# Kernel tuning notes

Hardware: AMD Instinct MI355X
Metric: run time of the kernel (lower is better)

The kernel has to match this reference:

```python
import jax, jax.numpy as jnp
import numpy as np
import math

S = 5   # num_states
D = 16  # observation_dim
F = 4   # transition_feature_dim
H = 2 * S  # transition net hidden


def setup_inputs() -> dict:
    key = jax.random.key(0)
    ks = jax.random.split(key, 10)
    B, T = 256, 4096
    observations = jax.random.normal(ks[0], (B, T, D), dtype=jnp.float32)
    transition_features = jax.random.normal(ks[1], (B, T, F), dtype=jnp.float32)
    # GaussianEmission params
    means = jax.random.normal(ks[2], (S, D), dtype=jnp.float32) * 0.1
    log_vars = jnp.zeros((S, D), dtype=jnp.float32)
    # HMM params
    log_initial = jnp.zeros((S,), dtype=jnp.float32)
    transition_bias = (jnp.eye(S) * 2.0 + jnp.ones((S, S)) * 0.1).astype(jnp.float32)
    # per-source-state transition nets: Linear(F,H)-Tanh-Linear(H,S)
    W1 = jax.random.normal(ks[3], (S, H, F), dtype=jnp.float32) * (1.0 / math.sqrt(F))
    b1 = jnp.zeros((S, H), dtype=jnp.float32)
    W2 = jax.random.normal(ks[4], (S, S, H), dtype=jnp.float32) * (1.0 / math.sqrt(H))
    b2 = jnp.zeros((S, S), dtype=jnp.float32)
    return {
        "observations": observations,
        "transition_features": transition_features,
        "means": means,
        "log_vars": log_vars,
        "log_initial": log_initial,
        "transition_bias": transition_bias,
        "W1": W1, "b1": b1, "W2": W2, "b2": b2,
    }


def _emission_log_prob(obs, means, log_vars):
    # diagonal Gaussian, expanded quadratic form to avoid [B,T,S,D] intermediate
    inv_v = jnp.exp(-log_vars)                              # [S,D]
    quad = (
        jnp.einsum('btd,sd->bts', obs * obs, inv_v)
        - 2.0 * jnp.einsum('btd,sd->bts', obs, means * inv_v)
        + jnp.sum(means * means * inv_v, axis=-1)           # [S]
    )
    const = D * math.log(2 * math.pi) + jnp.sum(log_vars, axis=-1)  # [S]
    return -0.5 * (const + quad)                            # [B,T,S]


def _io_log_transitions(feat, W1, b1, W2, b2, transition_bias):
    # feat: [B,T,F] -> log transition matrices [B,T,S,S] (row i = source state)
    h = jnp.tanh(jnp.einsum('btf,ihf->btih', feat, W1) + b1)        # [B,T,S,H]
    logits = jnp.einsum('btih,ioh->btio', h, W2) + b2 + transition_bias  # [B,T,S,S]
    probs = jax.nn.softmax(logits, axis=-1)
    return jnp.log(probs + 1e-10)


def reference(observations, transition_features, means, log_vars,
              log_initial, transition_bias, W1, b1, W2, b2):
    log_emis = _emission_log_prob(observations, means, log_vars)    # [B,T,S]
    log_init = jax.nn.log_softmax(log_initial)                      # [S]
    alpha0 = log_init + log_emis[:, 0, :]                           # [B,S]

    # transitions used at steps t=1..T-1
    log_trans = _io_log_transitions(transition_features[:, 1:], W1, b1, W2, b2,
                                    transition_bias)                # [B,T-1,S,S]

    lt_tm = jnp.swapaxes(log_trans, 0, 1)                           # [T-1,B,S,S]
    le_tm = jnp.swapaxes(log_emis[:, 1:, :], 0, 1)                  # [T-1,B,S]

    def step(alpha, xs):
        lt, le = xs
        alpha_new = jax.nn.logsumexp(alpha[:, :, None] + lt, axis=1) + le
        return alpha_new, alpha_new

    alpha_T, alphas = jax.lax.scan(step, alpha0, (lt_tm, le_tm))
    all_alpha = jnp.concatenate([alpha0[None], alphas], axis=0)     # [T,B,S]
    all_alpha = jnp.swapaxes(all_alpha, 0, 1)                       # [B,T,S]
    log_likelihood = jax.nn.logsumexp(alpha_T, axis=-1)             # [B]
    return log_likelihood, all_alpha
```

## Files before the change

### kernel.cpp

```cpp
#include <hip/hip_runtime.h>
#include <math.h>


namespace {

constexpr int kS = 5, kD = 16, kB = 256, kT = 4096;
constexpr int kC = 8, kNC = 512;
constexpr int kTile = 256, kCPT = 32;
constexpr int kG = 16, kNG = 32;

constexpr float kL2E = 1.4426950408889634f;
constexpr float kLn2 = 0.6931471805599453f;

constexpr int L_QA  = 0;
constexpr int L_QB  = 80;
constexpr int L_QC  = 160;
constexpr int L_LN  = 168;
constexpr int L_W1H = 176;
constexpr int L_B1  = 276;
constexpr int L_W2H = 336;
constexpr int P_TOT = 544;
constexpr int P_RSV = 1024;

typedef __fp16 half2_t __attribute__((ext_vector_type(2)));

#if __has_builtin(__builtin_amdgcn_exp2f)
__device__ __forceinline__ float ex2(float x) { return __builtin_amdgcn_exp2f(x); }
#else
__device__ __forceinline__ float ex2(float x) { return exp2f(x); }
#endif
#if __has_builtin(__builtin_amdgcn_logf)
__device__ __forceinline__ float lg2(float x) { return __builtin_amdgcn_logf(x); }
#else
__device__ __forceinline__ float lg2(float x) { return __log2f(x); }
#endif

__device__ __forceinline__ unsigned pkh(float a, float b) {
  return __builtin_bit_cast(unsigned, __builtin_amdgcn_cvt_pkrtz(a, b));
}

#if __has_builtin(__builtin_amdgcn_fdot2)
__device__ __forceinline__ float fdot2u(unsigned w, unsigned x, float acc) {
  return __builtin_amdgcn_fdot2(__builtin_bit_cast(half2_t, w),
                                __builtin_bit_cast(half2_t, x), acc, false);
}
#else
__device__ __forceinline__ float fdot2u(unsigned w, unsigned x, float acc) {
  const half2_t hw = __builtin_bit_cast(half2_t, w);
  const half2_t hx = __builtin_bit_cast(half2_t, x);
  return acc + (float)hw.x * (float)hx.x + (float)hw.y * (float)hx.y;
}
#endif

__device__ __forceinline__ float max5(float a0, float a1, float a2, float a3, float a4) {
  return fmaxf(fmaxf(fmaxf(a0, a1), fmaxf(a2, a3)), a4);
}

__device__ __forceinline__ unsigned bf16bits(float x) {
  unsigned u = __float_as_uint(x);
  return (u + 0x7fffu + ((u >> 16) & 1u)) >> 16;
}

__device__ __forceinline__ unsigned cvtpk(float a, float b) {
  unsigned r;
  asm("v_cvt_pk_bf16_f32 %0, %1, %2" : "=v"(r) : "v"(a), "v"(b));
  return r;
}

__device__ __forceinline__ int swcol(int row, int e) {
  return (e + 11 * (row >> 3) + (row & 7)) & 15;
}

__global__ void k_prep(const float* __restrict__ means, const float* __restrict__ lv,
                       const float* __restrict__ linit, const float* __restrict__ tbias,
                       const float* __restrict__ W1g, const float* __restrict__ b1g,
                       const float* __restrict__ W2g, const float* __restrict__ b2g,
                       float* __restrict__ P) {
  const int tid = threadIdx.x;
  if (tid < 80) {
    const float iv = __expf(-lv[tid]);
    P[L_QA + tid] = -0.5f * kL2E * iv;
    P[L_QB + tid] = kL2E * means[tid] * iv;
  }
  if (tid >= 80 && tid < 85) {
    const int s = tid - 80;
    float acc = 0.f;
#pragma unroll
    for (int d = 0; d < 16; ++d) {
      const float lvv = lv[s * 16 + d], mm = means[s * 16 + d];
      acc += lvv + mm * mm * __expf(-lvv);
    }
    P[L_QC + s] = -0.5f * kL2E * (29.406033062549525f + acc);
    const float l0 = linit[0], l1 = linit[1], l2 = linit[2], l3 = linit[3],
                l4 = linit[4];
    const float m = max5(l0, l1, l2, l3, l4);
    const float se = __expf(l0 - m) + __expf(l1 - m) + __expf(l2 - m) +
                     __expf(l3 - m) + __expf(l4 - m);
    P[L_LN + s] = kL2E * (linit[s] - (m + __logf(se)));
  }
  if (tid < 100) {
    const int i = tid / 20, rem = tid - i * 20, h = rem >> 1, part = rem & 1;
    const int base = (i * 10 + h) * 4 + part * 2;
    P[L_W1H + tid] = __uint_as_float(pkh((2.0f * kL2E) * W1g[base],
                                         (2.0f * kL2E) * W1g[base + 1]));
  }
  if (tid < 60) {
    const int r = tid / 12, h = tid - r * 12;
    P[L_B1 + tid] = (h < 10) ? (2.0f * kL2E) * b1g[r * 10 + h] : 0.f;
  }
  if (tid < 200) {
    const int r = tid >> 3, s = tid & 7;
    float v = 0.f;
    if (s < 5) {
      v = __uint_as_float(pkh(-2.0f * kL2E * W2g[r * 10 + 2 * s],
                              -2.0f * kL2E * W2g[r * 10 + 2 * s + 1]));
    } else if (s == 5) {
      float sw = 0.f;
#pragma unroll
      for (int hh = 0; hh < 10; ++hh) sw += W2g[r * 10 + hh];
      v = kL2E * (b2g[r] + tbias[r] + sw);
    }
    P[L_W2H + tid] = v;
  }
  if (tid < 3) { P[165 + tid] = 0.f; P[173 + tid] = 0.f; }
  if (tid < 8) P[536 + tid] = 0.f;
}

__device__ __forceinline__ void buildE(const float* __restrict__ obs,
                                       const float* __restrict__ feat,
                                       const float* __restrict__ p,
                                       size_t t, float E[25], float& c) {
  float o[16], o2[16];
  {
    const float4* o4 = reinterpret_cast<const float4*>(obs + t * kD);
    const float4 v0 = o4[0], v1 = o4[1], v2 = o4[2], v3 = o4[3];
    o[0] = v0.x; o[1] = v0.y; o[2] = v0.z; o[3] = v0.w;
    o[4] = v1.x; o[5] = v1.y; o[6] = v1.z; o[7] = v1.w;
    o[8] = v2.x; o[9] = v2.y; o[10] = v2.z; o[11] = v2.w;
    o[12] = v3.x; o[13] = v3.y; o[14] = v3.z; o[15] = v3.w;
  }
#pragma unroll
  for (int d = 0; d < 16; ++d) o2[d] = o[d] * o[d];
  float le[5];
#pragma unroll
  for (int s = 0; s < 5; ++s) {
    float acc = p[L_QC + s];
#pragma unroll
    for (int dq = 0; dq < 4; ++dq) {
      const float4 qa = *reinterpret_cast<const float4*>(p + L_QA + s * 16 + dq * 4);
      const float4 qb = *reinterpret_cast<const float4*>(p + L_QB + s * 16 + dq * 4);
      acc = fmaf(o2[dq * 4 + 0], qa.x, acc); acc = fmaf(o[dq * 4 + 0], qb.x, acc);
      acc = fmaf(o2[dq * 4 + 1], qa.y, acc); acc = fmaf(o[dq * 4 + 1], qb.y, acc);
      acc = fmaf(o2[dq * 4 + 2], qa.z, acc); acc = fmaf(o[dq * 4 + 2], qb.z, acc);
      acc = fmaf(o2[dq * 4 + 3], qa.w, acc); acc = fmaf(o[dq * 4 + 3], qb.w, acc);
    }
    le[s] = acc;
  }
  c = max5(le[0], le[1], le[2], le[3], le[4]);
  float eml[5];
#pragma unroll
  for (int j = 0; j < 5; ++j) eml[j] = ex2(le[j] - c);
  const float4 f = *reinterpret_cast<const float4*>(feat + t * 4);
  const unsigned f01 = pkh(f.x, f.y), f23 = pkh(f.z, f.w);
#pragma unroll
  for (int i = 0; i < 5; ++i) {
    const float4 bA = *reinterpret_cast<const float4*>(p + L_B1 + i * 12);
    const float4 bB = *reinterpret_cast<const float4*>(p + L_B1 + i * 12 + 4);
    const float2 bC = *reinterpret_cast<const float2*>(p + L_B1 + i * 12 + 8);
    const uint4 wa = *reinterpret_cast<const uint4*>(p + L_W1H + i * 20);
    const uint4 wb = *reinterpret_cast<const uint4*>(p + L_W1H + i * 20 + 4);
    const uint4 wc = *reinterpret_cast<const uint4*>(p + L_W1H + i * 20 + 8);
    const uint4 wd = *reinterpret_cast<const uint4*>(p + L_W1H + i * 20 + 12);
    const uint4 we = *reinterpret_cast<const uint4*>(p + L_W1H + i * 20 + 16);
    const float r0 = __builtin_amdgcn_rcpf(ex2(fdot2u(wa.y, f23, fdot2u(wa.x, f01, bA.x))) + 1.f);
    const float r1 = __builtin_amdgcn_rcpf(ex2(fdot2u(wa.w, f23, fdot2u(wa.z, f01, bA.y))) + 1.f);
    const float r2 = __builtin_amdgcn_rcpf(ex2(fdot2u(wb.y, f23, fdot2u(wb.x, f01, bA.z))) + 1.f);
    const float r3 = __builtin_amdgcn_rcpf(ex2(fdot2u(wb.w, f23, fdot2u(wb.z, f01, bA.w))) + 1.f);
    const float r4 = __builtin_amdgcn_rcpf(ex2(fdot2u(wc.y, f23, fdot2u(wc.x, f01, bB.x))) + 1.f);
    const float r5 = __builtin_amdgcn_rcpf(ex2(fdot2u(wc.w, f23, fdot2u(wc.z, f01, bB.y))) + 1.f);
    const float r6 = __builtin_amdgcn_rcpf(ex2(fdot2u(wd.y, f23, fdot2u(wd.x, f01, bB.z))) + 1.f);
    const float r7 = __builtin_amdgcn_rcpf(ex2(fdot2u(wd.w, f23, fdot2u(wd.z, f01, bB.w))) + 1.f);
    const float r8 = __builtin_amdgcn_rcpf(ex2(fdot2u(we.y, f23, fdot2u(we.x, f01, bC.x))) + 1.f);
    const float r9 = __builtin_amdgcn_rcpf(ex2(fdot2u(we.w, f23, fdot2u(we.z, f01, bC.y))) + 1.f);
    const unsigned h01 = pkh(r0, r1), h23 = pkh(r2, r3), h45 = pkh(r4, r5),
                   h67 = pkh(r6, r7), h89 = pkh(r8, r9);
    float eg[5], se = 0.f;
#pragma unroll
    for (int j = 0; j < 5; ++j) {
      const uint4 v = *reinterpret_cast<const uint4*>(p + L_W2H + (i * 5 + j) * 8);
      const uint2 v2 = *reinterpret_cast<const uint2*>(p + L_W2H + (i * 5 + j) * 8 + 4);
      float acc = __uint_as_float(v2.y);
      acc = fdot2u(v.x, h01, acc);
      acc = fdot2u(v.y, h23, acc);
      acc = fdot2u(v.z, h45, acc);
      acc = fdot2u(v.w, h67, acc);
      acc = fdot2u(v2.x, h89, acc);
      eg[j] = ex2(acc);
      se += eg[j];
    }
    const float rs = __builtin_amdgcn_rcpf(se);
#pragma unroll
    for (int j = 0; j < 5; ++j) E[i * 5 + j] = eg[j] * rs * eml[j];
  }
}

__device__ __forceinline__ void buildE0(const float* __restrict__ obs,
                                        const float* __restrict__ p, int b,
                                        float E[25], float& c) {
  float o[16], o2[16];
  {
    const float4* o4 = reinterpret_cast<const float4*>(obs + (size_t)b * kT * kD);
    const float4 v0 = o4[0], v1 = o4[1], v2 = o4[2], v3 = o4[3];
    o[0] = v0.x; o[1] = v0.y; o[2] = v0.z; o[3] = v0.w;
    o[4] = v1.x; o[5] = v1.y; o[6] = v1.z; o[7] = v1.w;
    o[8] = v2.x; o[9] = v2.y; o[10] = v2.z; o[11] = v2.w;
    o[12] = v3.x; o[13] = v3.y; o[14] = v3.z; o[15] = v3.w;
  }
#pragma unroll
  for (int d = 0; d < 16; ++d) o2[d] = o[d] * o[d];
  float v[5];
#pragma unroll
  for (int s = 0; s < 5; ++s) {
    float acc = p[L_QC + s];
#pragma unroll
    for (int dq = 0; dq < 4; ++dq) {
      const float4 qa = *reinterpret_cast<const float4*>(p + L_QA + s * 16 + dq * 4);
      const float4 qb = *reinterpret_cast<const float4*>(p + L_QB + s * 16 + dq * 4);
      acc = fmaf(o2[dq * 4 + 0], qa.x, acc); acc = fmaf(o[dq * 4 + 0], qb.x, acc);
      acc = fmaf(o2[dq * 4 + 1], qa.y, acc); acc = fmaf(o[dq * 4 + 1], qb.y, acc);
      acc = fmaf(o2[dq * 4 + 2], qa.z, acc); acc = fmaf(o[dq * 4 + 2], qb.z, acc);
      acc = fmaf(o2[dq * 4 + 3], qa.w, acc); acc = fmaf(o[dq * 4 + 3], qb.w, acc);
    }
    v[s] = acc + p[L_LN + s];
  }
  c = max5(v[0], v[1], v[2], v[3], v[4]);
  float e5[5];
#pragma unroll
  for (int j = 0; j < 5; ++j) e5[j] = 0.2f * ex2(v[j] - c);
#pragma unroll
  for (int i = 0; i < 5; ++i)
#pragma unroll
    for (int j = 0; j < 5; ++j) E[i * 5 + j] = e5[j];
}

template <bool STORE_E>
__global__ __launch_bounds__(kTile, 4) void k_build(
    const float* __restrict__ obs, const float* __restrict__ feat,
    const float* __restrict__ P, float* __restrict__ Rg,
    uint4* __restrict__ wsE) {
  __shared__ __align__(16) float p[P_TOT];
  __shared__ unsigned sw[kTile * 16];
  if (threadIdx.x < P_TOT / 4)
    reinterpret_cast<float4*>(p)[threadIdx.x] =
        reinterpret_cast<const float4*>(P)[threadIdx.x];
  __syncthreads();
  const int b = blockIdx.y, tile = blockIdx.x, tid = threadIdx.x;
  const int t = tile * kTile + tid;
  const size_t gt = (size_t)b * kT + t;
  float E[25], c;
  if (t == 0) buildE0(obs, p, b, E, c);
  else buildE(obs, feat, p, gt, E, c);
  unsigned w[14];
  w[0] = cvtpk(E[0], E[1]);   w[1] = cvtpk(E[2], E[3]);
  w[2] = cvtpk(E[4], E[5]);   w[3] = cvtpk(E[6], E[7]);
  w[4] = cvtpk(E[8], E[9]);   w[5] = cvtpk(E[10], E[11]);
  w[6] = cvtpk(E[12], E[13]); w[7] = cvtpk(E[14], E[15]);
  w[8] = cvtpk(E[16], E[17]); w[9] = cvtpk(E[18], E[19]);
  w[10] = cvtpk(E[20], E[21]); w[11] = cvtpk(E[22], E[23]);
  {
    const unsigned cb = __float_as_uint(c);
    w[12] = bf16bits(E[24]) | (cb << 16);
    w[13] = cb >> 16;
  }
  if (STORE_E) {
    uint4* wp = wsE + gt * 4;
    wp[0] = make_uint4(w[0], w[1], w[2], w[3]);
    wp[1] = make_uint4(w[4], w[5], w[6], w[7]);
    wp[2] = make_uint4(w[8], w[9], w[10], w[11]);
    wp[3] = make_uint4(w[12], w[13], 0u, 0u);
  }
  {
    const int base = tid * 16;
#pragma unroll
    for (int e = 0; e < 14; ++e) sw[base + swcol(tid, e)] = w[e];
  }
  __syncthreads();
  const int chunk = tid >> 3, ri = tid & 7;
  float R[5], sc;
  {
    const int row = chunk * 8, base = row * 16, cb = 11 * chunk;
#pragma unroll
    for (int m = 0; m < 5; ++m) {
      const int sl = ri * 5 + m, widx = sl >> 1;
      const unsigned d = sw[base + ((widx + cb) & 15)];
      R[m] = __uint_as_float((sl & 1) ? (d & 0xffff0000u) : (d << 16));
    }
    const unsigned d12 = sw[base + ((12 + cb) & 15)];
    const unsigned d13 = sw[base + ((13 + cb) & 15)];
    sc = __uint_as_float((d12 >> 16) | (d13 << 16));
  }
#pragma unroll 1
  for (int k = 1; k < 8; ++k) {
    const int row = chunk * 8 + k, base = row * 16, cb = 11 * chunk + k;
    unsigned d[14];
#pragma unroll
    for (int e = 0; e < 14; ++e) d[e] = sw[base + ((e + cb) & 15)];
    float Ek[25];
#pragma unroll
    for (int q = 0; q < 12; ++q) {
      Ek[2 * q]     = __uint_as_float(d[q] << 16);
      Ek[2 * q + 1] = __uint_as_float(d[q] & 0xffff0000u);
    }
    Ek[24] = __uint_as_float(d[12] << 16);
    sc += __uint_as_float((d[12] >> 16) | (d[13] << 16));
    float nR[5];
#pragma unroll
    for (int j = 0; j < 5; ++j) {
      float acc = R[0] * Ek[j];
      acc = fmaf(R[1], Ek[5 + j], acc);
      acc = fmaf(R[2], Ek[10 + j], acc);
      acc = fmaf(R[3], Ek[15 + j], acc);
      acc = fmaf(R[4], Ek[20 + j], acc);
      nR[j] = acc;
    }
#pragma unroll
    for (int j = 0; j < 5; ++j) R[j] = nR[j];
    if ((k & 1) == 0 || k == 7) {
      float rm = (ri < 5) ? max5(R[0], R[1], R[2], R[3], R[4]) : 0.f;
      rm = fmaxf(rm, __shfl_xor(rm, 1, 8));
      rm = fmaxf(rm, __shfl_xor(rm, 2, 8));
      rm = fmaxf(rm, __shfl_xor(rm, 4, 8));
      rm = fmaxf(rm, 1e-30f);
      const float r = __builtin_amdgcn_rcpf(rm);
#pragma unroll
      for (int j = 0; j < 5; ++j) R[j] *= r;
      sc += lg2(rm);
    }
  }
  if (ri < 5) {
    float* outr = Rg + ((size_t)b * kNC + tile * kCPT + chunk) * 28 + ri * 5;
#pragma unroll
    for (int m = 0; m < 5; ++m) outr[m] = R[m];
    if (ri == 0) outr[25] = sc;
  }
}


__device__ __forceinline__ void matmat5(float R[25], const float E[25]) {
#pragma unroll
  for (int i = 0; i < 5; ++i) {
    const float r0 = R[i * 5 + 0], r1 = R[i * 5 + 1], r2 = R[i * 5 + 2];
    const float r3 = R[i * 5 + 3], r4 = R[i * 5 + 4];
#pragma unroll
    for (int j = 0; j < 5; ++j) {
      float acc = r0 * E[j];
      acc = fmaf(r1, E[5 + j], acc);
      acc = fmaf(r2, E[10 + j], acc);
      acc = fmaf(r3, E[15 + j], acc);
      acc = fmaf(r4, E[20 + j], acc);
      R[i * 5 + j] = acc;
    }
  }
}

__device__ __forceinline__ void rescale25a(float R[25], float& sc) {
  float m = R[0];
#pragma unroll
  for (int e = 1; e < 25; ++e) m = fmaxf(m, R[e]);
  m = fmaxf(m, 1e-30f);
  const float r = __builtin_amdgcn_rcpf(m);
#pragma unroll
  for (int e = 0; e < 25; ++e) R[e] *= r;
  sc += lg2(m);
}

__device__ __forceinline__ void vecmat5(float a[5], const float M[25]) {
  float o[5];
#pragma unroll
  for (int j = 0; j < 5; ++j) {
    float acc = a[0] * M[j];
    acc = fmaf(a[1], M[5 + j], acc);
    acc = fmaf(a[2], M[10 + j], acc);
    acc = fmaf(a[3], M[15 + j], acc);
    acc = fmaf(a[4], M[20 + j], acc);
    o[j] = acc;
  }
#pragma unroll
  for (int j = 0; j < 5; ++j) a[j] = o[j];
}

__device__ __forceinline__ void rescale5(float a[5], float& ls) {
  const float m = fmaxf(max5(a[0], a[1], a[2], a[3], a[4]), 1e-30f);
  const float r = __builtin_amdgcn_rcpf(m);
#pragma unroll
  for (int j = 0; j < 5; ++j) a[j] *= r;
  ls += lg2(m);
}

__global__ __launch_bounds__(256) void k_scan(const float* __restrict__ Rg,
                                              float* __restrict__ start,
                                              float* __restrict__ out) {
  __shared__ float sR[kNC * 32];
  __shared__ float sP[kNG * 28];
  __shared__ float sA[kNG * 8];
  const int b = blockIdx.x, tid = threadIdx.x;
#pragma unroll
  for (int r = 0; r < 2; ++r) {
    const int rec = r * 256 + tid;
    const float4* src = reinterpret_cast<const float4*>(Rg + ((size_t)b * kNC + rec) * 28);
    float4 q[7];
#pragma unroll
    for (int i = 0; i < 7; ++i) q[i] = src[i];
    const float* v = reinterpret_cast<const float*>(q);
    const int base = rec * 32, off = rec + (rec >> 4);
#pragma unroll
    for (int e = 0; e < 26; ++e) sR[base + ((off + e) & 31)] = v[e];
  }
  __syncthreads();
  if (tid < kNG) {
    const int g = tid;
    float P[25], psc;
    {
      const int rec = g * kG, base = rec * 32, off = rec + (rec >> 4);
#pragma unroll
      for (int e = 0; e < 25; ++e) P[e] = sR[base + ((off + e) & 31)];
      psc = sR[base + ((off + 25) & 31)];
    }
#pragma unroll 1
    for (int k = 1; k < kG; ++k) {
      const int rec = g * kG + k, base = rec * 32, off = rec + (rec >> 4);
      float M[25];
#pragma unroll
      for (int e = 0; e < 25; ++e) M[e] = sR[base + ((off + e) & 31)];
      psc += sR[base + ((off + 25) & 31)];
      matmat5(P, M);
      if (k & 1) rescale25a(P, psc);
    }
#pragma unroll
    for (int e = 0; e < 25; ++e) sP[g * 28 + e] = P[e];
    sP[g * 28 + 25] = psc;
  }
  __syncthreads();
  if (tid == 0) {
    float a[5] = {1.f, 1.f, 1.f, 1.f, 1.f};
    float ls = 0.f;
#pragma unroll 1
    for (int g = 0; g < kNG; ++g) {
#pragma unroll
      for (int s = 0; s < 5; ++s) sA[g * 8 + s] = a[s];
      sA[g * 8 + 5] = ls;
      float M[25];
#pragma unroll
      for (int e = 0; e < 25; ++e) M[e] = sP[g * 28 + e];
      vecmat5(a, M);
      ls += sP[g * 28 + 25];
      rescale5(a, ls);
    }
    out[b] = (lg2(a[0] + a[1] + a[2] + a[3] + a[4]) + ls) * kLn2;
  }
  __syncthreads();
  if (tid < kNG) {
    const int g = tid;
    float a[5], ls;
#pragma unroll
    for (int s = 0; s < 5; ++s) a[s] = sA[g * 8 + s];
    ls = sA[g * 8 + 5];
#pragma unroll 1
    for (int k = 0; k < kG; ++k) {
      const int cc = g * kG + k;
      float* st = start + ((size_t)b * kNC + cc) * 8;
      reinterpret_cast<float4*>(st)[0] = make_float4(a[0], a[1], a[2], a[3]);
      reinterpret_cast<float4*>(st)[1] = make_float4(a[4], ls, 0.f, 0.f);
      const int base = cc * 32, off = cc + (cc >> 4);
      float M[25];
#pragma unroll
      for (int e = 0; e < 25; ++e) M[e] = sR[base + ((off + e) & 31)];
      ls += sR[base + ((off + 25) & 31)];
      vecmat5(a, M);
      rescale5(a, ls);
    }
  }
}

__global__ __launch_bounds__(256) void k_alpha_a(const uint4* __restrict__ wsE,
                                                 const float* __restrict__ start,
                                                 float* __restrict__ outp) {
  const int gc = blockIdx.x * 256 + threadIdx.x;
  const int b = gc >> 9, cc = gc & (kNC - 1);
  const float* st = start + (size_t)gc * 8;
  const float4 s0 = reinterpret_cast<const float4*>(st)[0];
  const float4 s1 = reinterpret_cast<const float4*>(st)[1];
  float a[5] = {s0.x, s0.y, s0.z, s0.w, s1.x};
  float ls = s1.y;
  float ov[40];
  const uint4* ep = wsE + ((size_t)b * kT + (size_t)cc * kC) * 4;
#pragma unroll
  for (int k = 0; k < 8; ++k) {
    uint4 q0 = ep[k * 4], q1 = ep[k * 4 + 1], q2 = ep[k * 4 + 2], q3 = ep[k * 4 + 3];
    unsigned d[14] = {q0.x, q0.y, q0.z, q0.w, q1.x, q1.y, q1.z, q1.w,
                      q2.x, q2.y, q2.z, q2.w, q3.x, q3.y};
    float E[25];
#pragma unroll
    for (int q = 0; q < 12; ++q) {
      E[2 * q]     = __uint_as_float(d[q] << 16);
      E[2 * q + 1] = __uint_as_float(d[q] & 0xffff0000u);
    }
    E[24] = __uint_as_float(d[12] << 16);
    const float cst = __uint_as_float((d[12] >> 16) | (d[13] << 16));
    float o[5];
#pragma unroll
    for (int j = 0; j < 5; ++j) {
      float acc = a[0] * E[j];
      acc = fmaf(a[1], E[5 + j], acc);
      acc = fmaf(a[2], E[10 + j], acc);
      acc = fmaf(a[3], E[15 + j], acc);
      acc = fmaf(a[4], E[20 + j], acc);
      o[j] = acc;
    }
    ls += cst;
    float L[5];
#pragma unroll
    for (int j = 0; j < 5; ++j) L[j] = lg2(o[j]);
#pragma unroll
    for (int j = 0; j < 5; ++j) ov[k * 5 + j] = (L[j] + ls) * kLn2;
    const float lm = max5(L[0], L[1], L[2], L[3], L[4]);
    const float m = fmaxf(max5(o[0], o[1], o[2], o[3], o[4]), 1e-30f);
    const float r = __builtin_amdgcn_rcpf(m);
#pragma unroll
    for (int j = 0; j < 5; ++j) a[j] = o[j] * r;
    ls += lm;
  }
  float4* w = reinterpret_cast<float4*>(outp + kB + ((size_t)b * kT + (size_t)cc * kC) * kS);
#pragma unroll
  for (int q = 0; q < 10; ++q)
    w[q] = make_float4(ov[q * 4], ov[q * 4 + 1], ov[q * 4 + 2], ov[q * 4 + 3]);
}

}

extern "C" void kernel_launch(void* const* d_in, const int* in_sizes, int n_in,
                              void* d_out, int out_size, void* d_ws, size_t ws_size,
                              hipStream_t stream) {
  (void)in_sizes; (void)n_in; (void)out_size; (void)ws_size;
  const float* obs   = (const float*)d_in[0];
  const float* feat  = (const float*)d_in[1];
  const float* means = (const float*)d_in[2];
  const float* lv    = (const float*)d_in[3];
  const float* linit = (const float*)d_in[4];
  const float* tbias = (const float*)d_in[5];
  const float* W1g   = (const float*)d_in[6];
  const float* b1g   = (const float*)d_in[7];
  const float* W2g   = (const float*)d_in[8];
  const float* b2g   = (const float*)d_in[9];
  float* out = (float*)d_out;

  float* P     = (float*)d_ws;
  float* Rg    = P + P_RSV;
  float* start = Rg + (size_t)kB * kNC * 28;
  uint4* wsE   = reinterpret_cast<uint4*>(start + (size_t)kB * kNC * 8);

  k_prep<<<1, 256, 0, stream>>>(means, lv, linit, tbias, W1g, b1g, W2g, b2g, P);
  dim3 gridB(kT / kTile, kB);
  k_build<true><<<gridB, kTile, 0, stream>>>(obs, feat, P, Rg, wsE);
  k_scan<<<kB, 256, 0, stream>>>(Rg, start, out);
  k_alpha_a<<<(kB * kNC) / 256, 256, 0, stream>>>(wsE, start, out);
}
```

Measured before the change: 108.3 us.

## Split alpha output chunks in half using stored mid-chunk transfer products

k_build now also writes the partial 4-step transfer product of each 8-step chunk to a new workspace buffer. k_alpha_a launches twice as many threads, each emitting 4 timesteps. Second-half threads jump to their start state with that stored half-chunk matrix, or by replaying 4 steps if workspace is too small. This shortens each thread's serial dependency chain and raises parallelism, at the cost of extra global writes in k_build and extra workspace.

```diff
diff --git a/kernel.cpp b/kernel.cpp
--- a/kernel.cpp
+++ b/kernel.cpp
@@ -247,7 +247,7 @@
 __global__ __launch_bounds__(kTile, 4) void k_build(
     const float* __restrict__ obs, const float* __restrict__ feat,
     const float* __restrict__ P, float* __restrict__ Rg,
-    uint4* __restrict__ wsE) {
+    uint4* __restrict__ wsE, float* __restrict__ Rhg) {
   __shared__ __align__(16) float p[P_TOT];
   __shared__ unsigned sw[kTile * 16];
   if (threadIdx.x < P_TOT / 4)
@@ -336,6 +336,12 @@
       for (int j = 0; j < 5; ++j) R[j] *= r;
       sc += lg2(rm);
     }
+    if (k == 3 && Rhg != nullptr && ri < 5) {
+      float* hr = Rhg + ((size_t)b * kNC + tile * kCPT + chunk) * 28 + ri * 5;
+#pragma unroll
+      for (int m = 0; m < 5; ++m) hr[m] = R[m];
+      if (ri == 0) hr[25] = sc;
+    }
   }
   if (ri < 5) {
     float* outr = Rg + ((size_t)b * kNC + tile * kCPT + chunk) * 28 + ri * 5;
@@ -395,6 +401,18 @@
 #pragma unroll
   for (int j = 0; j < 5; ++j) a[j] *= r;
   ls += lg2(m);
+}
+
+__device__ __forceinline__ void loadRec(const float* __restrict__ base, size_t rec,
+                                        float M[25], float& msc) {
+  const float4* src = reinterpret_cast<const float4*>(base + rec * 28);
+  float4 q[7];
+#pragma unroll
+  for (int i = 0; i < 7; ++i) q[i] = src[i];
+  const float* v = reinterpret_cast<const float*>(q);
+#pragma unroll
+  for (int e = 0; e < 25; ++e) M[e] = v[e];
+  msc = v[25];
 }
 
 __global__ __launch_bounds__(256) void k_scan(const float* __restrict__ Rg,
@@ -484,18 +502,50 @@
 
 __global__ __launch_bounds__(256) void k_alpha_a(const uint4* __restrict__ wsE,
                                                  const float* __restrict__ start,
+                                                 const float* __restrict__ Rhg,
                                                  float* __restrict__ outp) {
-  const int gc = blockIdx.x * 256 + threadIdx.x;
-  const int b = gc >> 9, cc = gc & (kNC - 1);
-  const float* st = start + (size_t)gc * 8;
+  const int gcc = blockIdx.x * 256 + threadIdx.x;
+  const int b = gcc >> 10;
+  const int rem = gcc & 1023;
+  const int h = rem >> 9;
+  const int cc = rem & 511;
+  const float* st = start + ((size_t)b * kNC + cc) * 8;
   const float4 s0 = reinterpret_cast<const float4*>(st)[0];
   const float4 s1 = reinterpret_cast<const float4*>(st)[1];
   float a[5] = {s0.x, s0.y, s0.z, s0.w, s1.x};
   float ls = s1.y;
-  float ov[40];
-  const uint4* ep = wsE + ((size_t)b * kT + (size_t)cc * kC) * 4;
-#pragma unroll
-  for (int k = 0; k < 8; ++k) {
+  if (h) {
+    if (Rhg != nullptr) {
+      float M[25], msc;
+      loadRec(Rhg, (size_t)b * kNC + cc, M, msc);
+      vecmat5(a, M);
+      ls += msc;
+      rescale5(a, ls);
+    } else {
+      const uint4* pp = wsE + ((size_t)b * kT + (size_t)cc * kC) * 4;
+#pragma unroll
+      for (int k = 0; k < 4; ++k) {
+        uint4 q0 = pp[k * 4], q1 = pp[k * 4 + 1], q2 = pp[k * 4 + 2], q3 = pp[k * 4 + 3];
+        unsigned d[14] = {q0.x, q0.y, q0.z, q0.w, q1.x, q1.y, q1.z, q1.w,
+                          q2.x, q2.y, q2.z, q2.w, q3.x, q3.y};
+        float E[25];
+#pragma unroll
+        for (int q = 0; q < 12; ++q) {
+          E[2 * q]     = __uint_as_float(d[q] << 16);
+          E[2 * q + 1] = __uint_as_float(d[q] & 0xffff0000u);
+        }
+        E[24] = __uint_as_float(d[12] << 16);
+        vecmat5(a, E);
+        ls += __uint_as_float((d[12] >> 16) | (d[13] << 16));
+        rescale5(a, ls);
+      }
+    }
+  }
+  const size_t t0 = (size_t)cc * kC + (size_t)h * 4;
+  float ov[20];
+  const uint4* ep = wsE + ((size_t)b * kT + t0) * 4;
+#pragma unroll
+  for (int k = 0; k < 4; ++k) {
     uint4 q0 = ep[k * 4], q1 = ep[k * 4 + 1], q2 = ep[k * 4 + 2], q3 = ep[k * 4 + 3];
     unsigned d[14] = {q0.x, q0.y, q0.z, q0.w, q1.x, q1.y, q1.z, q1.w,
                       q2.x, q2.y, q2.z, q2.w, q3.x, q3.y};
@@ -530,9 +580,9 @@
     for (int j = 0; j < 5; ++j) a[j] = o[j] * r;
     ls += lm;
   }
-  float4* w = reinterpret_cast<float4*>(outp + kB + ((size_t)b * kT + (size_t)cc * kC) * kS);
-#pragma unroll
-  for (int q = 0; q < 10; ++q)
+  float4* w = reinterpret_cast<float4*>(outp + kB + ((size_t)b * kT + t0) * kS);
+#pragma unroll
+  for (int q = 0; q < 5; ++q)
     w[q] = make_float4(ov[q * 4], ov[q * 4 + 1], ov[q * 4 + 2], ov[q * 4 + 3]);
 }
 
@@ -541,7 +591,7 @@
 extern "C" void kernel_launch(void* const* d_in, const int* in_sizes, int n_in,
                               void* d_out, int out_size, void* d_ws, size_t ws_size,
                               hipStream_t stream) {
-  (void)in_sizes; (void)n_in; (void)out_size; (void)ws_size;
+  (void)in_sizes; (void)n_in; (void)out_size;
   const float* obs   = (const float*)d_in[0];
   const float* feat  = (const float*)d_in[1];
   const float* means = (const float*)d_in[2];
@@ -558,10 +608,15 @@
   float* Rg    = P + P_RSV;
   float* start = Rg + (size_t)kB * kNC * 28;
   uint4* wsE   = reinterpret_cast<uint4*>(start + (size_t)kB * kNC * 8);
+  float* Rhf   = reinterpret_cast<float*>(wsE) + (size_t)kB * kT * 16;
+  const size_t needB = ((size_t)P_RSV + (size_t)kB * kNC * 28 +
+                        (size_t)kB * kNC * 8 + (size_t)kB * kNC * 28) * 4 +
+                       (size_t)kB * kT * 64;
+  float* Rhg = (ws_size >= needB) ? Rhf : nullptr;
 
   k_prep<<<1, 256, 0, stream>>>(means, lv, linit, tbias, W1g, b1g, W2g, b2g, P);
   dim3 gridB(kT / kTile, kB);
-  k_build<true><<<gridB, kTile, 0, stream>>>(obs, feat, P, Rg, wsE);
+  k_build<true><<<gridB, kTile, 0, stream>>>(obs, feat, P, Rg, wsE, Rhg);
   k_scan<<<kB, 256, 0, stream>>>(Rg, start, out);
-  k_alpha_a<<<(kB * kNC) / 256, 256, 0, stream>>>(wsE, start, out);
-}
+  k_alpha_a<<<(kB * kNC * 2) / 256, 256, 0, stream>>>(wsE, start, Rhg, out);
+}
```

Result: slower. 117.0 us (+8.1%).

## Reduce each chunk's 5x5 transition products in one thread with doubled tiles

Applied to the files above, without the earlier changes.

The tile size goes from 256 to 512 timesteps, and chunks per tile go from 32 to 64. The per-chunk product of 8 emission-transition matrices changes mapping: before, 8 lanes each carried one row and shared a max via shuffles; now a single thread holds the full 5x5 matrix and rescales it with a local max. Results go out as contiguous float4 stores. This removes the cross-lane shuffles and the idle lanes (3 of every 8), but only 64 of 512 threads do the reduction phase, each with about five times the serial work. The larger register footprint under __launch_bounds__(512,4) also risks spills.

```diff
diff --git a/kernel.cpp b/kernel.cpp
--- a/kernel.cpp
+++ b/kernel.cpp
@@ -6,7 +6,7 @@
 
 constexpr int kS = 5, kD = 16, kB = 256, kT = 4096;
 constexpr int kC = 8, kNC = 512;
-constexpr int kTile = 256, kCPT = 32;
+constexpr int kTile = 512, kCPT = 64;
 constexpr int kG = 16, kNG = 32;
 
 constexpr float kL2E = 1.4426950408889634f;
@@ -69,6 +69,58 @@
 
 __device__ __forceinline__ int swcol(int row, int e) {
   return (e + 11 * (row >> 3) + (row & 7)) & 15;
+}
+
+
+__device__ __forceinline__ void matmat5(float R[25], const float E[25]) {
+#pragma unroll
+  for (int i = 0; i < 5; ++i) {
+    const float r0 = R[i * 5 + 0], r1 = R[i * 5 + 1], r2 = R[i * 5 + 2];
+    const float r3 = R[i * 5 + 3], r4 = R[i * 5 + 4];
+#pragma unroll
+    for (int j = 0; j < 5; ++j) {
+      float acc = r0 * E[j];
+      acc = fmaf(r1, E[5 + j], acc);
+      acc = fmaf(r2, E[10 + j], acc);
+      acc = fmaf(r3, E[15 + j], acc);
+      acc = fmaf(r4, E[20 + j], acc);
+      R[i * 5 + j] = acc;
+    }
+  }
+}
+
+__device__ __forceinline__ void rescale25a(float R[25], float& sc) {
+  float m = R[0];
+#pragma unroll
+  for (int e = 1; e < 25; ++e) m = fmaxf(m, R[e]);
+  m = fmaxf(m, 1e-30f);
+  const float r = __builtin_amdgcn_rcpf(m);
+#pragma unroll
+  for (int e = 0; e < 25; ++e) R[e] *= r;
+  sc += lg2(m);
+}
+
+__device__ __forceinline__ void vecmat5(float a[5], const float M[25]) {
+  float o[5];
+#pragma unroll
+  for (int j = 0; j < 5; ++j) {
+    float acc = a[0] * M[j];
+    acc = fmaf(a[1], M[5 + j], acc);
+    acc = fmaf(a[2], M[10 + j], acc);
+    acc = fmaf(a[3], M[15 + j], acc);
+    acc = fmaf(a[4], M[20 + j], acc);
+    o[j] = acc;
+  }
+#pragma unroll
+  for (int j = 0; j < 5; ++j) a[j] = o[j];
+}
+
+__device__ __forceinline__ void rescale5(float a[5], float& ls) {
+  const float m = fmaxf(max5(a[0], a[1], a[2], a[3], a[4]), 1e-30f);
+  const float r = __builtin_amdgcn_rcpf(m);
+#pragma unroll
+  for (int j = 0; j < 5; ++j) a[j] *= r;
+  ls += lg2(m);
 }
 
 __global__ void k_prep(const float* __restrict__ means, const float* __restrict__ lv,
@@ -257,144 +309,89 @@
   const int b = blockIdx.y, tile = blockIdx.x, tid = threadIdx.x;
   const int t = tile * kTile + tid;
   const size_t gt = (size_t)b * kT + t;
-  float E[25], c;
-  if (t == 0) buildE0(obs, p, b, E, c);
-  else buildE(obs, feat, p, gt, E, c);
-  unsigned w[14];
-  w[0] = cvtpk(E[0], E[1]);   w[1] = cvtpk(E[2], E[3]);
-  w[2] = cvtpk(E[4], E[5]);   w[3] = cvtpk(E[6], E[7]);
-  w[4] = cvtpk(E[8], E[9]);   w[5] = cvtpk(E[10], E[11]);
-  w[6] = cvtpk(E[12], E[13]); w[7] = cvtpk(E[14], E[15]);
-  w[8] = cvtpk(E[16], E[17]); w[9] = cvtpk(E[18], E[19]);
-  w[10] = cvtpk(E[20], E[21]); w[11] = cvtpk(E[22], E[23]);
   {
-    const unsigned cb = __float_as_uint(c);
-    w[12] = bf16bits(E[24]) | (cb << 16);
-    w[13] = cb >> 16;
-  }
-  if (STORE_E) {
-    uint4* wp = wsE + gt * 4;
-    wp[0] = make_uint4(w[0], w[1], w[2], w[3]);
-    wp[1] = make_uint4(w[4], w[5], w[6], w[7]);
-    wp[2] = make_uint4(w[8], w[9], w[10], w[11]);
-    wp[3] = make_uint4(w[12], w[13], 0u, 0u);
-  }
-  {
+    float E[25], c;
+    if (t == 0) buildE0(obs, p, b, E, c);
+    else buildE(obs, feat, p, gt, E, c);
+    unsigned w[14];
+    w[0] = cvtpk(E[0], E[1]);   w[1] = cvtpk(E[2], E[3]);
+    w[2] = cvtpk(E[4], E[5]);   w[3] = cvtpk(E[6], E[7]);
+    w[4] = cvtpk(E[8], E[9]);   w[5] = cvtpk(E[10], E[11]);
+    w[6] = cvtpk(E[12], E[13]); w[7] = cvtpk(E[14], E[15]);
+    w[8] = cvtpk(E[16], E[17]); w[9] = cvtpk(E[18], E[19]);
+    w[10] = cvtpk(E[20], E[21]); w[11] = cvtpk(E[22], E[23]);
+    {
+      const unsigned cb = __float_as_uint(c);
+      w[12] = bf16bits(E[24]) | (cb << 16);
+      w[13] = cb >> 16;
+    }
+    if (STORE_E) {
+      uint4* wp = wsE + gt * 4;
+      wp[0] = make_uint4(w[0], w[1], w[2], w[3]);
+      wp[1] = make_uint4(w[4], w[5], w[6], w[7]);
+      wp[2] = make_uint4(w[8], w[9], w[10], w[11]);
+      wp[3] = make_uint4(w[12], w[13], 0u, 0u);
+    }
     const int base = tid * 16;
 #pragma unroll
     for (int e = 0; e < 14; ++e) sw[base + swcol(tid, e)] = w[e];
   }
   __syncthreads();
-  const int chunk = tid >> 3, ri = tid & 7;
-  float R[5], sc;
-  {
-    const int row = chunk * 8, base = row * 16, cb = 11 * chunk;
-#pragma unroll
-    for (int m = 0; m < 5; ++m) {
-      const int sl = ri * 5 + m, widx = sl >> 1;
-      const unsigned d = sw[base + ((widx + cb) & 15)];
-      R[m] = __uint_as_float((sl & 1) ? (d & 0xffff0000u) : (d << 16));
-    }
-    const unsigned d12 = sw[base + ((12 + cb) & 15)];
-    const unsigned d13 = sw[base + ((13 + cb) & 15)];
-    sc = __uint_as_float((d12 >> 16) | (d13 << 16));
-  }
+  if (tid < kCPT) {
+    const int c = tid;
+    float R[25], sc;
+    {
+      const int base = (c * 8) * 16, cb = 11 * c;
+      unsigned d[14];
+#pragma unroll
+      for (int e = 0; e < 14; ++e) d[e] = sw[base + ((e + cb) & 15)];
+#pragma unroll
+      for (int q = 0; q < 12; ++q) {
+        R[2 * q]     = __uint_as_float(d[q] << 16);
+        R[2 * q + 1] = __uint_as_float(d[q] & 0xffff0000u);
+      }
+      R[24] = __uint_as_float(d[12] << 16);
+      sc = __uint_as_float((d[12] >> 16) | (d[13] << 16));
+    }
 #pragma unroll 1
-  for (int k = 1; k < 8; ++k) {
-    const int row = chunk * 8 + k, base = row * 16, cb = 11 * chunk + k;
-    unsigned d[14];
-#pragma unroll
-    for (int e = 0; e < 14; ++e) d[e] = sw[base + ((e + cb) & 15)];
-    float Ek[25];
-#pragma unroll
-    for (int q = 0; q < 12; ++q) {
-      Ek[2 * q]     = __uint_as_float(d[q] << 16);
-      Ek[2 * q + 1] = __uint_as_float(d[q] & 0xffff0000u);
-    }
-    Ek[24] = __uint_as_float(d[12] << 16);
-    sc += __uint_as_float((d[12] >> 16) | (d[13] << 16));
-    float nR[5];
-#pragma unroll
-    for (int j = 0; j < 5; ++j) {
-      float acc = R[0] * Ek[j];
-      acc = fmaf(R[1], Ek[5 + j], acc);
-      acc = fmaf(R[2], Ek[10 + j], acc);
-      acc = fmaf(R[3], Ek[15 + j], acc);
-      acc = fmaf(R[4], Ek[20 + j], acc);
-      nR[j] = acc;
-    }
-#pragma unroll
-    for (int j = 0; j < 5; ++j) R[j] = nR[j];
-    if ((k & 1) == 0 || k == 7) {
-      float rm = (ri < 5) ? max5(R[0], R[1], R[2], R[3], R[4]) : 0.f;
-      rm = fmaxf(rm, __shfl_xor(rm, 1, 8));
-      rm = fmaxf(rm, __shfl_xor(rm, 2, 8));
-      rm = fmaxf(rm, __shfl_xor(rm, 4, 8));
-      rm = fmaxf(rm, 1e-30f);
-      const float r = __builtin_amdgcn_rcpf(rm);
-#pragma unroll
-      for (int j = 0; j < 5; ++j) R[j] *= r;
-      sc += lg2(rm);
-    }
-  }
-  if (ri < 5) {
-    float* outr = Rg + ((size_t)b * kNC + tile * kCPT + chunk) * 28 + ri * 5;
-#pragma unroll
-    for (int m = 0; m < 5; ++m) outr[m] = R[m];
-    if (ri == 0) outr[25] = sc;
-  }
-}
-
-
-__device__ __forceinline__ void matmat5(float R[25], const float E[25]) {
-#pragma unroll
-  for (int i = 0; i < 5; ++i) {
-    const float r0 = R[i * 5 + 0], r1 = R[i * 5 + 1], r2 = R[i * 5 + 2];
-    const float r3 = R[i * 5 + 3], r4 = R[i * 5 + 4];
-#pragma unroll
-    for (int j = 0; j < 5; ++j) {
-      float acc = r0 * E[j];
-      acc = fmaf(r1, E[5 + j], acc);
-      acc = fmaf(r2, E[10 + j], acc);
-      acc = fmaf(r3, E[15 + j], acc);
-      acc = fmaf(r4, E[20 + j], acc);
-      R[i * 5 + j] = acc;
-    }
-  }
-}
-
-__device__ __forceinline__ void rescale25a(float R[25], float& sc) {
-  float m = R[0];
-#pragma unroll
-  for (int e = 1; e < 25; ++e) m = fmaxf(m, R[e]);
-  m = fmaxf(m, 1e-30f);
-  const float r = __builtin_amdgcn_rcpf(m);
-#pragma unroll
-  for (int e = 0; e < 25; ++e) R[e] *= r;
-  sc += lg2(m);
-}
-
-__device__ __forceinline__ void vecmat5(float a[5], const float M[25]) {
-  float o[5];
-#pragma unroll
-  for (int j = 0; j < 5; ++j) {
-    float acc = a[0] * M[j];
-    acc = fmaf(a[1], M[5 + j], acc);
-    acc = fmaf(a[2], M[10 + j], acc);
-    acc = fmaf(a[3], M[15 + j], acc);
-    acc = fmaf(a[4], M[20 + j], acc);
-    o[j] = acc;
-  }
-#pragma unroll
-  for (int j = 0; j < 5; ++j) a[j] = o[j];
-}
-
-__device__ __forceinline__ void rescale5(float a[5], float& ls) {
-  const float m = fmaxf(max5(a[0], a[1], a[2], a[3], a[4]), 1e-30f);
-  const float r = __builtin_amdgcn_rcpf(m);
-#pragma unroll
-  for (int j = 0; j < 5; ++j) a[j] *= r;
-  ls += lg2(m);
+    for (int k = 1; k < 8; ++k) {
+      const int base = (c * 8 + k) * 16, cb = 11 * c + k;
+      unsigned d[14];
+#pragma unroll
+      for (int e = 0; e < 14; ++e) d[e] = sw[base + ((e + cb) & 15)];
+      float Ek[25];
+#pragma unroll
+      for (int q = 0; q < 12; ++q) {
+        Ek[2 * q]     = __uint_as_float(d[q] << 16);
+        Ek[2 * q + 1] = __uint_as_float(d[q] & 0xffff0000u);
+      }
+      Ek[24] = __uint_as_float(d[12] << 16);
+      sc += __uint_as_float((d[12] >> 16) | (d[13] << 16));
+      matmat5(R, Ek);
+      if (k & 1) rescale25a(R, sc);
+    }
+    float4* o4 = reinterpret_cast<float4*>(
+        Rg + ((size_t)b * kNC + tile * kCPT + c) * 28);
+    o4[0] = make_float4(R[0], R[1], R[2], R[3]);
+    o4[1] = make_float4(R[4], R[5], R[6], R[7]);
+    o4[2] = make_float4(R[8], R[9], R[10], R[11]);
+    o4[3] = make_float4(R[12], R[13], R[14], R[15]);
+    o4[4] = make_float4(R[16], R[17], R[18], R[19]);
+    o4[5] = make_float4(R[20], R[21], R[22], R[23]);
+    o4[6] = make_float4(R[24], sc, 0.f, 0.f);
+  }
+}
+
+__device__ __forceinline__ void loadRec(const float* __restrict__ base, size_t rec,
+                                        float M[25], float& msc) {
+  const float4* src = reinterpret_cast<const float4*>(base + rec * 28);
+  float4 q[7];
+#pragma unroll
+  for (int i = 0; i < 7; ++i) q[i] = src[i];
+  const float* v = reinterpret_cast<const float*>(q);
+#pragma unroll
+  for (int e = 0; e < 25; ++e) M[e] = v[e];
+  msc = v[25];
 }
 
 __global__ __launch_bounds__(256) void k_scan(const float* __restrict__ Rg,
```

New measurement: 111.3 us. 2.9% more time.
